# Kernel tuning notes

Hardware: AMD Instinct MI355X
Metric: run time of the kernel (lower is better)

Reference implementation:

```python
import jax, jax.numpy as jnp
import numpy as np

B, S, H = 512, 200, 256

def setup_inputs() -> dict:
    key = jax.random.key(0)
    ks = jax.random.split(key, 7)
    scale = 1.0 / np.sqrt(H)
    return {
        "all_memory": jax.random.normal(ks[0], (B, S, H), dtype=jnp.float32),
        "last_memory": jax.random.normal(ks[1], (B, H), dtype=jnp.float32),
        "U": jax.random.normal(ks[2], (H, H), dtype=jnp.float32) * scale,   # U_meta weight
        "W": jax.random.normal(ks[3], (H, H), dtype=jnp.float32) * scale,   # W_meta weight
        "V": jax.random.normal(ks[4], (H, 1), dtype=jnp.float32) * scale,   # V_meta weight (stored as [H,1])
        "MetaW": jax.random.normal(ks[5], (4, H), dtype=jnp.float32) * scale,  # Meta weight
        "Metab": jax.random.normal(ks[6], (4,), dtype=jnp.float32) * scale,    # Meta bias ('multiple' mode)
    }

def reference(all_memory, last_memory, U, W, V, MetaW, Metab):
    # U_meta(all_memory): [B,S,H]; W_meta(last_memory): [B,H] broadcast over S
    a = jnp.einsum('bsh,kh->bsk', all_memory, U)
    l = jnp.einsum('bh,kh->bk', last_memory, W)
    # additive attention score: V_meta(tanh(a + l)) -> [B,S]
    scores = jnp.einsum('bsh,h->bs', jnp.tanh(a + l[:, None, :]), V[:, 0])
    alpha = jax.nn.softmax(scores, axis=1)  # softmax over seq dim
    pooled = jnp.einsum('bs,bsh->bh', alpha, all_memory)  # weighted sum of values
    return pooled @ MetaW.T + Metab  # [B, 4]
```

## Files before the change

### kernel.cpp

```cpp
#include <hip/hip_runtime.h>
#include <hip/hip_bf16.h>
#include <math.h>

#define NB 512
#define NS 200
#define NH 256
#define TILE_S 32

#define OFF_L    0
#define OFF_UB   (NB * NH)
#define WS_FLOATS_PRE  (OFF_UB + (NH * NH) / 2)

typedef _Float16 f16x8 __attribute__((ext_vector_type(8)));
typedef float    f32x4 __attribute__((ext_vector_type(4)));

#define SWZ(r, u) ((((u) ^ ((r) & 7))) * 8)

template<int CTRL>
__device__ __forceinline__ float dpp_xadd(float v) {
  return v + __int_as_float(
      __builtin_amdgcn_update_dpp(0, __float_as_int(v), CTRL, 0xf, 0xf, true));
}
__device__ __forceinline__ float row16_sum(float v) {
  v = dpp_xadd<0xB1>(v);
  v = dpp_xadd<0x4E>(v);
  v = dpp_xadd<0x124>(v);
  v = dpp_xadd<0x128>(v);
  return v;
}

__global__ __launch_bounds__(256)
void precompute(const float* __restrict__ lastm, const float* __restrict__ W,
                const float* __restrict__ U,
                float* __restrict__ l_ws, _Float16* __restrict__ Uswz)
{
  const int t = threadIdx.x;
  if (blockIdx.x < NB) {
    const int b = blockIdx.x;
    __shared__ float lm_sm[NH];
    lm_sm[t] = lastm[(size_t)b * NH + t];
    __syncthreads();
    const float4* wrow = (const float4*)(W + (size_t)t * NH);
    const float4* lrow = (const float4*)lm_sm;
    float a0 = 0.f, a1 = 0.f, a2 = 0.f, a3 = 0.f;
#pragma unroll 8
    for (int i = 0; i < NH / 4; ++i) {
      float4 w4 = wrow[i];
      float4 m4 = lrow[i];
      a0 = fmaf(w4.x, m4.x, a0);
      a1 = fmaf(w4.y, m4.y, a1);
      a2 = fmaf(w4.z, m4.z, a2);
      a3 = fmaf(w4.w, m4.w, a3);
    }
    l_ws[(size_t)b * NH + t] = (a0 + a1) + (a2 + a3);
  } else {
    const int id    = (blockIdx.x - NB) * 256 + t;
    const int n_blk = id >> 9;
    const int kk    = (id >> 6) & 7;
    const int lane  = id & 63;
    const int row   = n_blk * 16 + (lane & 15);
    const int col   = kk * 32 + (lane >> 4) * 8;
    const float4* s = (const float4*)(U + (size_t)row * NH + col);
    const float4 a = s[0], c = s[1];
    f16x8 pk;
    pk[0] = (_Float16)a.x; pk[1] = (_Float16)a.y;
    pk[2] = (_Float16)a.z; pk[3] = (_Float16)a.w;
    pk[4] = (_Float16)c.x; pk[5] = (_Float16)c.y;
    pk[6] = (_Float16)c.z; pk[7] = (_Float16)c.w;
    *(f16x8*)(Uswz + (size_t)id * 8) = pk;
  }
}

#define CVT_HL(idx, val) { const float x_ = (val); const _Float16 h_ = (_Float16)x_; \
                           ph[idx] = h_; pl[idx] = (_Float16)(x_ - (float)h_); }

template<bool PRE>
__global__ __launch_bounds__(512, 2)
void fused_attn(const float* __restrict__ mem,
                const float* __restrict__ lastm,
                const float* __restrict__ U,
                const float* __restrict__ W,
                const float* __restrict__ V,
                const float* __restrict__ l_ws,
                const _Float16* __restrict__ Uswz,
                const float* __restrict__ MetaW,
                const float* __restrict__ Metab,
                float* __restrict__ out)
{
  const int b = blockIdx.x;

  const int t     = threadIdx.x;
  const int wave  = t >> 6;
  const int lane  = t & 63;
  const int m16   = lane & 15;
  const int quad  = lane >> 4;
  const int g     = t >> 5;
  const int u31   = t & 31;

  __shared__ __align__(16) _Float16 hi_sm[2][TILE_S][NH];
  __shared__ __align__(16) _Float16 lo_sm[2][TILE_S][NH];
  __shared__ float swave_sm[8][TILE_S];
  __shared__ float e_sm[TILE_S];
  __shared__ float z_sm[1];

  float l_reg[2], v_reg[2];
  if constexpr (!PRE) {
    __shared__ float l_sm[NH];
    __shared__ float lm_sm[NH];
    if (t < NH) lm_sm[t] = lastm[(size_t)b * NH + t];
    __syncthreads();
    if (t < NH) {
      const float4* wrow = (const float4*)(W + (size_t)t * NH);
      const float4* lrow = (const float4*)lm_sm;
      float a0 = 0.f, a1 = 0.f, a2 = 0.f, a3 = 0.f;
#pragma unroll 8
      for (int i = 0; i < NH / 4; ++i) {
        float4 w4 = wrow[i];
        float4 m4 = lrow[i];
        a0 = fmaf(w4.x, m4.x, a0);
        a1 = fmaf(w4.y, m4.y, a1);
        a2 = fmaf(w4.z, m4.z, a2);
        a3 = fmaf(w4.w, m4.w, a3);
      }
      l_sm[t] = (a0 + a1) + (a2 + a3);
    }
    __syncthreads();
#pragma unroll
    for (int nf = 0; nf < 2; ++nf)
      l_reg[nf] = l_sm[wave * 32 + nf * 16 + m16];
  } else {
#pragma unroll
    for (int nf = 0; nf < 2; ++nf)
      l_reg[nf] = l_ws[(size_t)b * NH + wave * 32 + nf * 16 + m16];
  }
#pragma unroll
  for (int nf = 0; nf < 2; ++nf)
    v_reg[nf] = V[wave * 32 + nf * 16 + m16];
  const float vsum  = v_reg[0] + v_reg[1];
  const float vm2_0 = -2.f * v_reg[0];
  const float vm2_1 = -2.f * v_reg[1];

  f16x8 u_frag[2][8];
  if constexpr (PRE) {
    const _Float16* uw = Uswz + ((size_t)(wave * 2 * 8 * 64) + lane) * 8;
#pragma unroll
    for (int nf = 0; nf < 2; ++nf)
#pragma unroll
      for (int kk = 0; kk < 8; ++kk)
        u_frag[nf][kk] = *(const f16x8*)(uw + (size_t)((nf * 8 + kk) << 9));
  } else {
#pragma unroll
    for (int nf = 0; nf < 2; ++nf) {
      const int n = wave * 32 + nf * 16 + m16;
      const float* urow = U + (size_t)n * NH;
#pragma unroll
      for (int kk = 0; kk < 8; ++kk) {
        const float4 lo = *(const float4*)(urow + kk * 32 + quad * 8);
        const float4 hi = *(const float4*)(urow + kk * 32 + quad * 8 + 4);
        f16x8 f;
        f[0] = (_Float16)lo.x; f[1] = (_Float16)lo.y;
        f[2] = (_Float16)lo.z; f[3] = (_Float16)lo.w;
        f[4] = (_Float16)hi.x; f[5] = (_Float16)hi.y;
        f[6] = (_Float16)hi.z; f[7] = (_Float16)hi.w;
        u_frag[nf][kk] = f;
      }
    }
  }

  float4 q00, q01, q10, q11;
  {
    const float4* src4 = (const float4*)(mem + (size_t)b * NS * NH);
    const int r0 = t >> 5, r1 = 16 + (t >> 5);
    const float4 a0 = src4[t * 2],         a1 = src4[t * 2 + 1];
    const float4 b0 = src4[(512 + t) * 2], b1 = src4[(512 + t) * 2 + 1];
    {
      f16x8 ph, pl;
      CVT_HL(0, a0.x) CVT_HL(1, a0.y) CVT_HL(2, a0.z) CVT_HL(3, a0.w)
      CVT_HL(4, a1.x) CVT_HL(5, a1.y) CVT_HL(6, a1.z) CVT_HL(7, a1.w)
      *(f16x8*)&hi_sm[0][r0][SWZ(r0, u31)] = ph;
      *(f16x8*)&lo_sm[0][r0][SWZ(r0, u31)] = pl;
    }
    {
      f16x8 ph, pl;
      CVT_HL(0, b0.x) CVT_HL(1, b0.y) CVT_HL(2, b0.z) CVT_HL(3, b0.w)
      CVT_HL(4, b1.x) CVT_HL(5, b1.y) CVT_HL(6, b1.z) CVT_HL(7, b1.w)
      *(f16x8*)&hi_sm[0][r1][SWZ(r1, u31)] = ph;
      *(f16x8*)&lo_sm[0][r1][SWZ(r1, u31)] = pl;
    }
    const float4* nsrc = (const float4*)(mem + ((size_t)b * NS + TILE_S) * NH);
    q00 = nsrc[t * 2];         q01 = nsrc[t * 2 + 1];
    q10 = nsrc[(512 + t) * 2]; q11 = nsrc[(512 + t) * 2 + 1];
  }
  __syncthreads();

  float z_local = 0.f;
  float pooledv[8];
#pragma unroll
  for (int j = 0; j < 8; ++j) pooledv[j] = 0.f;

  for (int tile = 0; tile < 6; ++tile) {
    const int cur = tile & 1;
    const int nxt = cur ^ 1;
    const int s0  = tile * TILE_S;
    const int rows_w = min(TILE_S, NS - (s0 + TILE_S));
    const int rows_i = (tile + 2 < 7) ? min(TILE_S, NS - (s0 + 2 * TILE_S)) : 0;

    f32x4 acc[2][2];
    const f32x4 fzero = {0.f, 0.f, 0.f, 0.f};
#pragma unroll
    for (int mt = 0; mt < 2; ++mt)
#pragma unroll
      for (int nf = 0; nf < 2; ++nf)
        acc[mt][nf] = fzero;

#pragma unroll
    for (int kk = 0; kk < 8; ++kk) {
      const int c = SWZ(m16, kk * 4 + quad);
      f16x8 a0h = *(const f16x8*)&hi_sm[cur][m16][c];
      f16x8 a1h = *(const f16x8*)&hi_sm[cur][16 + m16][c];
      f16x8 a0l = *(const f16x8*)&lo_sm[cur][m16][c];
      f16x8 a1l = *(const f16x8*)&lo_sm[cur][16 + m16][c];
#pragma unroll
      for (int nf = 0; nf < 2; ++nf) {
        acc[0][nf] = __builtin_amdgcn_mfma_f32_16x16x32_f16(a0h, u_frag[nf][kk], acc[0][nf], 0, 0, 0);
        acc[1][nf] = __builtin_amdgcn_mfma_f32_16x16x32_f16(a1h, u_frag[nf][kk], acc[1][nf], 0, 0, 0);
        acc[0][nf] = __builtin_amdgcn_mfma_f32_16x16x32_f16(a0l, u_frag[nf][kk], acc[0][nf], 0, 0, 0);
        acc[1][nf] = __builtin_amdgcn_mfma_f32_16x16x32_f16(a1l, u_frag[nf][kk], acc[1][nf], 0, 0, 0);
      }
    }

#pragma unroll
    for (int mt = 0; mt < 2; ++mt) {
#pragma unroll
      for (int reg = 0; reg < 4; ++reg) {
        const float x0 = acc[mt][0][reg] + l_reg[0];
        const float x1 = acc[mt][1][reg] + l_reg[1];
        const float e0 = __expf(x0 + x0);
        const float e1 = __expf(x1 + x1);
        float s = vsum;
        s += __fdividef(vm2_0, e0 + 1.f);
        s += __fdividef(vm2_1, e1 + 1.f);
        s = row16_sum(s);
        if (m16 == 0)
          swave_sm[wave][mt * 16 + quad * 4 + reg] = s;
      }
    }
    __syncthreads();

    if (t < TILE_S) {
      float s = swave_sm[0][t];
#pragma unroll
      for (int w = 1; w < 8; ++w) s += swave_sm[w][t];
      const float e = __expf(s);
      e_sm[t] = e;
      z_local += e;
    }

    if ((t >> 5) < rows_w) {
      const int r = t >> 5;
      f16x8 ph, pl;
      CVT_HL(0, q00.x) CVT_HL(1, q00.y) CVT_HL(2, q00.z) CVT_HL(3, q00.w)
      CVT_HL(4, q01.x) CVT_HL(5, q01.y) CVT_HL(6, q01.z) CVT_HL(7, q01.w)
      *(f16x8*)&hi_sm[nxt][r][SWZ(r, u31)] = ph;
      *(f16x8*)&lo_sm[nxt][r][SWZ(r, u31)] = pl;
    }
    if (16 + (t >> 5) < rows_w) {
      const int r = 16 + (t >> 5);
      f16x8 ph, pl;
      CVT_HL(0, q10.x) CVT_HL(1, q10.y) CVT_HL(2, q10.z) CVT_HL(3, q10.w)
      CVT_HL(4, q11.x) CVT_HL(5, q11.y) CVT_HL(6, q11.z) CVT_HL(7, q11.w)
      *(f16x8*)&hi_sm[nxt][r][SWZ(r, u31)] = ph;
      *(f16x8*)&lo_sm[nxt][r][SWZ(r, u31)] = pl;
    }

    if (rows_i > 0) {
      const float4* nsrc = (const float4*)(mem + ((size_t)b * NS + s0 + 2 * TILE_S) * NH);
      if ((t >> 5) < rows_i)      { q00 = nsrc[t * 2];         q01 = nsrc[t * 2 + 1]; }
      if (16 + (t >> 5) < rows_i) { q10 = nsrc[(512 + t) * 2]; q11 = nsrc[(512 + t) * 2 + 1]; }
    }
    __syncthreads();

    const float e0 = e_sm[2 * g];
    const float e1 = e_sm[2 * g + 1];
    const f16x8 r0 = *(const f16x8*)&hi_sm[cur][2 * g][SWZ(2 * g, u31)];
    const f16x8 r1 = *(const f16x8*)&hi_sm[cur][2 * g + 1][SWZ(2 * g + 1, u31)];
#pragma unroll
    for (int j = 0; j < 8; ++j)
      pooledv[j] = fmaf(e0, (float)r0[j], fmaf(e1, (float)r1[j], pooledv[j]));
  }

  {
    f32x4 acc[2];
    const f32x4 fzero = {0.f, 0.f, 0.f, 0.f};
    acc[0] = fzero; acc[1] = fzero;
#pragma unroll
    for (int kk = 0; kk < 8; ++kk) {
      const int c = SWZ(m16, kk * 4 + quad);
      f16x8 a0h = *(const f16x8*)&hi_sm[0][m16][c];
      f16x8 a0l = *(const f16x8*)&lo_sm[0][m16][c];
#pragma unroll
      for (int nf = 0; nf < 2; ++nf) {
        acc[nf] = __builtin_amdgcn_mfma_f32_16x16x32_f16(a0h, u_frag[nf][kk], acc[nf], 0, 0, 0);
        acc[nf] = __builtin_amdgcn_mfma_f32_16x16x32_f16(a0l, u_frag[nf][kk], acc[nf], 0, 0, 0);
      }
    }
#pragma unroll
    for (int reg = 0; reg < 4; ++reg) {
      const float x0 = acc[0][reg] + l_reg[0];
      const float x1 = acc[1][reg] + l_reg[1];
      const float e0 = __expf(x0 + x0);
      const float e1 = __expf(x1 + x1);
      float s = vsum;
      s += __fdividef(vm2_0, e0 + 1.f);
      s += __fdividef(vm2_1, e1 + 1.f);
      s = row16_sum(s);
      if (m16 == 0)
        swave_sm[wave][quad * 4 + reg] = s;
    }
    __syncthreads();

    if (t < TILE_S) {
      float e = 0.f;
      if (t < 8) {
        float s = swave_sm[0][t];
#pragma unroll
        for (int w = 1; w < 8; ++w) s += swave_sm[w][t];
        e = __expf(s);
      }
      e_sm[t] = e;
      z_local += e;
    }
    __syncthreads();

    const float e0 = e_sm[2 * g];
    const float e1 = e_sm[2 * g + 1];
    const f16x8 r0 = *(const f16x8*)&hi_sm[0][2 * g][SWZ(2 * g, u31)];
    const f16x8 r1 = *(const f16x8*)&hi_sm[0][2 * g + 1][SWZ(2 * g + 1, u31)];
#pragma unroll
    for (int j = 0; j < 8; ++j)
      pooledv[j] = fmaf(e0, (float)r0[j], fmaf(e1, (float)r1[j], pooledv[j]));
  }
  __syncthreads();

  float* scratch   = (float*)&hi_sm[0][0][0];
  float* pooled_sm = (float*)&lo_sm[0][0][0];
  if (t < TILE_S) {
    float z = z_local;
#pragma unroll
    for (int off = 1; off < 32; off <<= 1)
      z += __shfl_xor(z, off);
    if (t == 0) z_sm[0] = z;
  }
  {
    const int hblk = u31 * 8;
    f32x4 lo4 = {pooledv[0], pooledv[1], pooledv[2], pooledv[3]};
    f32x4 hi4 = {pooledv[4], pooledv[5], pooledv[6], pooledv[7]};
    *(f32x4*)&scratch[g * 264 + hblk]     = lo4;
    *(f32x4*)&scratch[g * 264 + hblk + 4] = hi4;
  }
  __syncthreads();
  const float Zi = 1.f / z_sm[0];
  if (t < NH) {
    float p = 0.f;
#pragma unroll
    for (int r = 0; r < 16; ++r)
      p += scratch[r * 264 + t];
    pooled_sm[t] = p * Zi;
  }
  __syncthreads();
  if (t < 256) {
    float s = 0.f;
#pragma unroll
    for (int i = 0; i < 4; ++i) {
      const int h = i * 64 + lane;
      s = fmaf(pooled_sm[h], MetaW[(size_t)wave * NH + h], s);
    }
#pragma unroll
    for (int off = 32; off > 0; off >>= 1)
      s += __shfl_down(s, off);
    if (lane == 0)
      out[b * 4 + wave] = s + Metab[wave];
  }
}

extern "C" void kernel_launch(void* const* d_in, const int* in_sizes, int n_in,
                              void* d_out, int out_size, void* d_ws, size_t ws_size,
                              hipStream_t stream) {
  const float* mem   = (const float*)d_in[0];
  const float* lastm = (const float*)d_in[1];
  const float* U     = (const float*)d_in[2];
  const float* W     = (const float*)d_in[3];
  const float* V     = (const float*)d_in[4];
  const float* MetaW = (const float*)d_in[5];
  const float* Metab = (const float*)d_in[6];
  float* out = (float*)d_out;
  float* ws  = (float*)d_ws;

  if (ws_size >= (size_t)WS_FLOATS_PRE * sizeof(float)) {
    float*    l_ws = ws + OFF_L;
    _Float16* Uswz = (_Float16*)(ws + OFF_UB);
    hipLaunchKernelGGL(precompute, dim3(NB + 32), dim3(256), 0, stream,
                       lastm, W, U, l_ws, Uswz);
    hipLaunchKernelGGL(fused_attn<true>, dim3(NB), dim3(512), 0, stream,
                       mem, lastm, U, W, V, l_ws, Uswz, MetaW, Metab, out);
  } else {
    hipLaunchKernelGGL(fused_attn<false>, dim3(NB), dim3(512), 0, stream,
                       mem, lastm, U, W, V, (const float*)nullptr, (const _Float16*)nullptr,
                       MetaW, Metab, out);
  }
}
```

Baseline: 192.2 us.

## Drop precompute kernel and fuse l projection into attention kernel with early loads

Removes the separate precompute launch that produced W·last_memory and a swizzled fp16 copy of U in workspace. The fused kernel now always computes the l projection per block and converts U to fp16 fragments inline. The first two memory tiles are loaded before that work so their latency overlaps it. This saves a kernel launch and a workspace round trip. In exchange every block redoes the 256x256 W matvec and reads U in fp32, and more registers stay live early.

```diff
diff --git a/kernel.cpp b/kernel.cpp
--- a/kernel.cpp
+++ b/kernel.cpp
@@ -6,10 +6,6 @@
 #define NS 200
 #define NH 256
 #define TILE_S 32
-
-#define OFF_L    0
-#define OFF_UB   (NB * NH)
-#define WS_FLOATS_PRE  (OFF_UB + (NH * NH) / 2)
 
 typedef _Float16 f16x8 __attribute__((ext_vector_type(8)));
 typedef float    f32x4 __attribute__((ext_vector_type(4)));
@@ -29,60 +25,15 @@
   return v;
 }
 
-__global__ __launch_bounds__(256)
-void precompute(const float* __restrict__ lastm, const float* __restrict__ W,
-                const float* __restrict__ U,
-                float* __restrict__ l_ws, _Float16* __restrict__ Uswz)
-{
-  const int t = threadIdx.x;
-  if (blockIdx.x < NB) {
-    const int b = blockIdx.x;
-    __shared__ float lm_sm[NH];
-    lm_sm[t] = lastm[(size_t)b * NH + t];
-    __syncthreads();
-    const float4* wrow = (const float4*)(W + (size_t)t * NH);
-    const float4* lrow = (const float4*)lm_sm;
-    float a0 = 0.f, a1 = 0.f, a2 = 0.f, a3 = 0.f;
-#pragma unroll 8
-    for (int i = 0; i < NH / 4; ++i) {
-      float4 w4 = wrow[i];
-      float4 m4 = lrow[i];
-      a0 = fmaf(w4.x, m4.x, a0);
-      a1 = fmaf(w4.y, m4.y, a1);
-      a2 = fmaf(w4.z, m4.z, a2);
-      a3 = fmaf(w4.w, m4.w, a3);
-    }
-    l_ws[(size_t)b * NH + t] = (a0 + a1) + (a2 + a3);
-  } else {
-    const int id    = (blockIdx.x - NB) * 256 + t;
-    const int n_blk = id >> 9;
-    const int kk    = (id >> 6) & 7;
-    const int lane  = id & 63;
-    const int row   = n_blk * 16 + (lane & 15);
-    const int col   = kk * 32 + (lane >> 4) * 8;
-    const float4* s = (const float4*)(U + (size_t)row * NH + col);
-    const float4 a = s[0], c = s[1];
-    f16x8 pk;
-    pk[0] = (_Float16)a.x; pk[1] = (_Float16)a.y;
-    pk[2] = (_Float16)a.z; pk[3] = (_Float16)a.w;
-    pk[4] = (_Float16)c.x; pk[5] = (_Float16)c.y;
-    pk[6] = (_Float16)c.z; pk[7] = (_Float16)c.w;
-    *(f16x8*)(Uswz + (size_t)id * 8) = pk;
-  }
-}
-
 #define CVT_HL(idx, val) { const float x_ = (val); const _Float16 h_ = (_Float16)x_; \
                            ph[idx] = h_; pl[idx] = (_Float16)(x_ - (float)h_); }
 
-template<bool PRE>
 __global__ __launch_bounds__(512, 2)
 void fused_attn(const float* __restrict__ mem,
                 const float* __restrict__ lastm,
                 const float* __restrict__ U,
                 const float* __restrict__ W,
                 const float* __restrict__ V,
-                const float* __restrict__ l_ws,
-                const _Float16* __restrict__ Uswz,
                 const float* __restrict__ MetaW,
                 const float* __restrict__ Metab,
                 float* __restrict__ out)
@@ -102,77 +53,69 @@
   __shared__ float swave_sm[8][TILE_S];
   __shared__ float e_sm[TILE_S];
   __shared__ float z_sm[1];
+  __shared__ float l_sm[NH];
+  __shared__ float lm_sm[NH];
+
+  float4 a0, a1, b0, b1;
+  float4 q00, q01, q10, q11;
+  {
+    const float4* src4 = (const float4*)(mem + (size_t)b * NS * NH);
+    a0 = src4[t * 2];         a1 = src4[t * 2 + 1];
+    b0 = src4[(512 + t) * 2]; b1 = src4[(512 + t) * 2 + 1];
+    const float4* nsrc = (const float4*)(mem + ((size_t)b * NS + TILE_S) * NH);
+    q00 = nsrc[t * 2];         q01 = nsrc[t * 2 + 1];
+    q10 = nsrc[(512 + t) * 2]; q11 = nsrc[(512 + t) * 2 + 1];
+  }
+
+  if (t < NH) lm_sm[t] = lastm[(size_t)b * NH + t];
+  __syncthreads();
+  if (t < NH) {
+    const float4* wrow = (const float4*)(W + (size_t)t * NH);
+    const float4* lrow = (const float4*)lm_sm;
+    float c0 = 0.f, c1 = 0.f, c2 = 0.f, c3 = 0.f;
+#pragma unroll 8
+    for (int i = 0; i < NH / 4; ++i) {
+      float4 w4 = wrow[i];
+      float4 m4 = lrow[i];
+      c0 = fmaf(w4.x, m4.x, c0);
+      c1 = fmaf(w4.y, m4.y, c1);
+      c2 = fmaf(w4.z, m4.z, c2);
+      c3 = fmaf(w4.w, m4.w, c3);
+    }
+    l_sm[t] = (c0 + c1) + (c2 + c3);
+  }
+  __syncthreads();
 
   float l_reg[2], v_reg[2];
-  if constexpr (!PRE) {
-    __shared__ float l_sm[NH];
-    __shared__ float lm_sm[NH];
-    if (t < NH) lm_sm[t] = lastm[(size_t)b * NH + t];
-    __syncthreads();
-    if (t < NH) {
-      const float4* wrow = (const float4*)(W + (size_t)t * NH);
-      const float4* lrow = (const float4*)lm_sm;
-      float a0 = 0.f, a1 = 0.f, a2 = 0.f, a3 = 0.f;
-#pragma unroll 8
-      for (int i = 0; i < NH / 4; ++i) {
-        float4 w4 = wrow[i];
-        float4 m4 = lrow[i];
-        a0 = fmaf(w4.x, m4.x, a0);
-        a1 = fmaf(w4.y, m4.y, a1);
-        a2 = fmaf(w4.z, m4.z, a2);
-        a3 = fmaf(w4.w, m4.w, a3);
-      }
-      l_sm[t] = (a0 + a1) + (a2 + a3);
-    }
-    __syncthreads();
-#pragma unroll
-    for (int nf = 0; nf < 2; ++nf)
-      l_reg[nf] = l_sm[wave * 32 + nf * 16 + m16];
-  } else {
-#pragma unroll
-    for (int nf = 0; nf < 2; ++nf)
-      l_reg[nf] = l_ws[(size_t)b * NH + wave * 32 + nf * 16 + m16];
-  }
-#pragma unroll
-  for (int nf = 0; nf < 2; ++nf)
+#pragma unroll
+  for (int nf = 0; nf < 2; ++nf) {
+    l_reg[nf] = l_sm[wave * 32 + nf * 16 + m16];
     v_reg[nf] = V[wave * 32 + nf * 16 + m16];
+  }
   const float vsum  = v_reg[0] + v_reg[1];
   const float vm2_0 = -2.f * v_reg[0];
   const float vm2_1 = -2.f * v_reg[1];
 
   f16x8 u_frag[2][8];
-  if constexpr (PRE) {
-    const _Float16* uw = Uswz + ((size_t)(wave * 2 * 8 * 64) + lane) * 8;
-#pragma unroll
-    for (int nf = 0; nf < 2; ++nf)
-#pragma unroll
-      for (int kk = 0; kk < 8; ++kk)
-        u_frag[nf][kk] = *(const f16x8*)(uw + (size_t)((nf * 8 + kk) << 9));
-  } else {
-#pragma unroll
-    for (int nf = 0; nf < 2; ++nf) {
-      const int n = wave * 32 + nf * 16 + m16;
-      const float* urow = U + (size_t)n * NH;
-#pragma unroll
-      for (int kk = 0; kk < 8; ++kk) {
-        const float4 lo = *(const float4*)(urow + kk * 32 + quad * 8);
-        const float4 hi = *(const float4*)(urow + kk * 32 + quad * 8 + 4);
-        f16x8 f;
-        f[0] = (_Float16)lo.x; f[1] = (_Float16)lo.y;
-        f[2] = (_Float16)lo.z; f[3] = (_Float16)lo.w;
-        f[4] = (_Float16)hi.x; f[5] = (_Float16)hi.y;
-        f[6] = (_Float16)hi.z; f[7] = (_Float16)hi.w;
-        u_frag[nf][kk] = f;
-      }
-    }
-  }
-
-  float4 q00, q01, q10, q11;
+#pragma unroll
+  for (int nf = 0; nf < 2; ++nf) {
+    const int n = wave * 32 + nf * 16 + m16;
+    const float* urow = U + (size_t)n * NH;
+#pragma unroll
+    for (int kk = 0; kk < 8; ++kk) {
+      const float4 lo = *(const float4*)(urow + kk * 32 + quad * 8);
+      const float4 hi = *(const float4*)(urow + kk * 32 + quad * 8 + 4);
+      f16x8 f;
+      f[0] = (_Float16)lo.x; f[1] = (_Float16)lo.y;
+      f[2] = (_Float16)lo.z; f[3] = (_Float16)lo.w;
+      f[4] = (_Float16)hi.x; f[5] = (_Float16)hi.y;
+      f[6] = (_Float16)hi.z; f[7] = (_Float16)hi.w;
+      u_frag[nf][kk] = f;
+    }
+  }
+
   {
-    const float4* src4 = (const float4*)(mem + (size_t)b * NS * NH);
     const int r0 = t >> 5, r1 = 16 + (t >> 5);
-    const float4 a0 = src4[t * 2],         a1 = src4[t * 2 + 1];
-    const float4 b0 = src4[(512 + t) * 2], b1 = src4[(512 + t) * 2 + 1];
     {
       f16x8 ph, pl;
       CVT_HL(0, a0.x) CVT_HL(1, a0.y) CVT_HL(2, a0.z) CVT_HL(3, a0.w)
@@ -187,9 +130,6 @@
       *(f16x8*)&hi_sm[0][r1][SWZ(r1, u31)] = ph;
       *(f16x8*)&lo_sm[0][r1][SWZ(r1, u31)] = pl;
     }
-    const float4* nsrc = (const float4*)(mem + ((size_t)b * NS + TILE_S) * NH);
-    q00 = nsrc[t * 2];         q01 = nsrc[t * 2 + 1];
-    q10 = nsrc[(512 + t) * 2]; q11 = nsrc[(512 + t) * 2 + 1];
   }
   __syncthreads();
 
@@ -394,18 +334,8 @@
   const float* MetaW = (const float*)d_in[5];
   const float* Metab = (const float*)d_in[6];
   float* out = (float*)d_out;
-  float* ws  = (float*)d_ws;
-
-  if (ws_size >= (size_t)WS_FLOATS_PRE * sizeof(float)) {
-    float*    l_ws = ws + OFF_L;
-    _Float16* Uswz = (_Float16*)(ws + OFF_UB);
-    hipLaunchKernelGGL(precompute, dim3(NB + 32), dim3(256), 0, stream,
-                       lastm, W, U, l_ws, Uswz);
-    hipLaunchKernelGGL(fused_attn<true>, dim3(NB), dim3(512), 0, stream,
-                       mem, lastm, U, W, V, l_ws, Uswz, MetaW, Metab, out);
-  } else {
-    hipLaunchKernelGGL(fused_attn<false>, dim3(NB), dim3(512), 0, stream,
-                       mem, lastm, U, W, V, (const float*)nullptr, (const _Float16*)nullptr,
-                       MetaW, Metab, out);
-  }
+  (void)d_ws; (void)ws_size;
+
+  hipLaunchKernelGGL(fused_attn, dim3(NB), dim3(512), 0, stream,
+                     mem, lastm, U, W, V, MetaW, Metab, out);
 }
```

Result: slower. 211.9 us (+10.2%).
